# Kernel optimization log

Hardware: AMD Instinct MI355X
Metric: run time of the kernel (lower is better)

## Reference

```python
import jax, jax.numpy as jnp
import numpy as np

N = 100000
E = 6400000
GAMMA = 1.0
SUPPORT = 0.05


def cohesion_kernel(q, h):
    # piecewise Akinci cohesion kernel (Cd normalization is unused in the original)
    qm1_3_q3 = (q - 1.0) ** 3 * q ** 3
    k1 = 128.0 * qm1_3_q3 + 1.0   # q <= 0.5
    k2 = 64.0 * qm1_3_q3           # q > 0.5
    return -jnp.where(q <= 0.5, k1, k2)


def kernel_gradient(q, dist, h):
    # 2D Wendland C2 kernel gradient: W = 7/(pi h^2) (1-q)^4 (1+4q)
    C = 7.0 / (np.pi * h ** 2)
    dWdq = C * (-20.0 * q * jnp.clip(1.0 - q, 0.0, None) ** 3) / h
    return dWdq[:, None] * dist  # [E,2]


def setup_inputs() -> dict:
    key = jax.random.key(0)
    k1, k2, k3, k4, k5, k6, k7 = jax.random.split(key, 7)
    neighbors = jnp.stack([
        jax.random.randint(k1, (E,), 0, N),
        jax.random.randint(k2, (E,), 0, N),
    ], axis=0)  # [2,E] int
    fluidAreas = jax.random.uniform(k3, (N,), dtype=jnp.float32)
    fluidDensities = jax.random.uniform(k4, (N,), dtype=jnp.float32) + 0.5  # avoid div-by-0
    fluidRestDensity = jax.random.uniform(k5, (N,), dtype=jnp.float32) + 0.5
    fluidRadialDistances = jax.random.uniform(k6, (E,), dtype=jnp.float32)  # q in [0,1]
    fluidDistances = jax.random.normal(k7, (E, 2), dtype=jnp.float32)
    # normalize to unit direction vectors as in the SPH pipeline
    fluidDistances = fluidDistances / (jnp.linalg.norm(fluidDistances, axis=1, keepdims=True) + 1e-7)
    return {
        'neighbors': neighbors,
        'fluidAreas': fluidAreas,
        'fluidDensities': fluidDensities,
        'fluidRestDensity': fluidRestDensity,
        'fluidRadialDistances': fluidRadialDistances,
        'fluidDistances': fluidDistances,
    }


def reference(neighbors, fluidAreas, fluidDensities, fluidRestDensity,
              fluidRadialDistances, fluidDistances):
    i = neighbors[0]
    j = neighbors[1]

    # computeNormalFunction
    fac_n = fluidAreas[j] / fluidDensities[j]                  # [E]
    grad = kernel_gradient(fluidRadialDistances, fluidDistances, SUPPORT)  # [E,2]
    normals = SUPPORT * jax.ops.segment_sum(fac_n[:, None] * grad, i, num_segments=N)  # [N,2]

    # computeCurvatureForce
    curvature = -GAMMA * jax.ops.segment_sum(normals[i] - normals[j], i, num_segments=N)

    # computeCohesionForce
    fac_c = fluidAreas[j] * fluidRestDensity[j]                # [E]
    kern = cohesion_kernel(fluidRadialDistances, SUPPORT)      # [E]
    cohesion = -GAMMA * jax.ops.segment_sum((fac_c * kern)[:, None] * fluidDistances, i, num_segments=N)

    # both forces are accumulated into fluidAcceleration
    return curvature + cohesion
```

## Files before the change

### kernel.cpp

```cpp
#include <hip/hip_runtime.h>

constexpr int N_PART = 100000;
constexpr int N_EDGE = 6400000;
constexpr float SUPPORT = 0.05f;
constexpr float PI_F = 3.14159265358979323846f;

constexpr int CH_LOG2 = 12;
constexpr int CH      = 1 << CH_LOG2;
constexpr int NCH     = (N_EDGE + CH - 1) / CH;
constexpr int BIN_LOG2 = 13;
constexpr int BINSZ   = 1 << BIN_LOG2;
constexpr int NBIN    = (N_PART + BINSZ - 1) / BINSZ;
constexpr int G_MAX   = 39;
constexpr int ST_NW   = 8;

__global__ __launch_bounds__(512) void l1_sort(
    const int* __restrict__ nb,
    const float* __restrict__ areas,
    const float* __restrict__ dens,
    const float* __restrict__ rest,
    const float* __restrict__ q,
    const float2* __restrict__ dist,
    unsigned* __restrict__ gpack,
    float2* __restrict__ gpay1,
    float2* __restrict__ gpay2,
    unsigned* __restrict__ btab)
{
    __shared__ unsigned rec_pack[CH];
    __shared__ float    rec_q[CH];
    __shared__ float    rec_dx[CH];
    __shared__ float    rec_dy[CH];
    __shared__ unsigned hist[ST_NW * NBIN];
    __shared__ unsigned curw[ST_NW * NBIN];
    __shared__ unsigned base[NBIN + 1];

    const int t   = blockIdx.x;
    const int c0  = t * CH;
    const int len = min(CH, N_EDGE - c0);
    const int tid = threadIdx.x;
    const int wid = tid >> 6;

    for (int k = tid; k < ST_NW * NBIN; k += 512) hist[k] = 0u;
    __syncthreads();

    for (int idx = tid; idx < len; idx += 512) {
        unsigned i = (unsigned)nb[c0 + idx];
        atomicAdd(&hist[wid * NBIN + (i >> BIN_LOG2)], 1u);
    }
    __syncthreads();

    if (tid == 0) {
        unsigned run = 0;
        for (int b = 0; b < NBIN; ++b) {
            base[b] = run;
            for (int w = 0; w < ST_NW; ++w) {
                curw[w * NBIN + b] = run;
                run += hist[w * NBIN + b];
            }
        }
        base[NBIN] = run;
    }
    __syncthreads();
    if (tid < NBIN)  btab[t * 16 + tid]  = base[tid];
    if (tid == NBIN) btab[t * 16 + NBIN] = (unsigned)len;

    for (int idx = tid; idx < len; idx += 512) {
        unsigned i = (unsigned)nb[c0 + idx];
        unsigned j = (unsigned)nb[N_EDGE + c0 + idx];
        float   qq = q[c0 + idx];
        float2  d  = dist[c0 + idx];
        unsigned bin = i >> BIN_LOG2;
        unsigned r = atomicAdd(&curw[wid * NBIN + bin], 1u) & (CH - 1);
        rec_pack[r] = ((i & (BINSZ - 1)) << 17) | j;
        rec_q[r]    = qq;
        rec_dx[r]   = d.x;
        rec_dy[r]   = d.y;
    }
    __syncthreads();

    const float Cw = 7.0f / (PI_F * SUPPORT * SUPPORT);
    for (int p = tid; p < len; p += 512) {
        unsigned pack = rec_pack[p];
        float qq = rec_q[p];
        float dx = rec_dx[p], dy = rec_dy[p];
        unsigned j = pack & 0x1FFFFu;

        float omq  = fmaxf(1.0f - qq, 0.0f);
        float dWdq = Cw * (-20.0f * qq * omq * omq * omq) * (1.0f / SUPPORT);
        float s    = SUPPORT * (areas[j] / dens[j]) * dWdq;

        float qm1  = qq - 1.0f;
        float tt   = qm1 * qm1 * qm1 * qq * qq * qq;
        float kern = (qq <= 0.5f) ? fmaf(128.0f, tt, 1.0f) : 64.0f * tt;
        float fc   = areas[j] * rest[j] * kern;

        int o = c0 + p;
        gpack[o] = pack;
        gpay1[o] = make_float2(s * dx, s * dy);
        gpay2[o] = make_float2(fc * dx, fc * dy);
    }
}

__global__ __launch_bounds__(512) void passB(
    const unsigned* __restrict__ btab,
    const unsigned* __restrict__ gpack,
    const float2* __restrict__ gpay1,
    float2* __restrict__ partials,
    int G)
{
    __shared__ float accx[BINSZ];
    __shared__ float accy[BINSZ];
    const int b = blockIdx.x % NBIN;
    const int g = blockIdx.x / NBIN;
    const int wave = threadIdx.x >> 6;
    const int lane = threadIdx.x & 63;

    for (int k = threadIdx.x; k < BINSZ; k += 512) { accx[k] = 0.0f; accy[k] = 0.0f; }
    __syncthreads();

    const int t0 = (int)((long long)g * NCH / G);
    const int t1 = (int)((long long)(g + 1) * NCH / G);
    for (int t = t0 + wave; t < t1; t += 8) {
        const int c0  = t * CH;
        const unsigned ln = min(btab[t * 16 + NBIN], (unsigned)CH);
        unsigned sb = min(btab[t * 16 + b], ln);
        unsigned se = min(btab[t * 16 + b + 1], ln);
        for (unsigned k = sb + lane; k < se; k += 64) {
            int o = c0 + (int)k;
            unsigned pk = gpack[o];
            float2 p = gpay1[o];
            unsigned loc = (pk >> 17) & (BINSZ - 1);
            atomicAdd(&accx[loc], p.x);
            atomicAdd(&accy[loc], p.y);
        }
    }
    __syncthreads();

    float2* __restrict__ dst = partials + (size_t)g * (NBIN * BINSZ) + (size_t)b * BINSZ;
    for (int k = threadIdx.x; k < BINSZ; k += 512)
        dst[k] = make_float2(accx[k], accy[k]);
}

__global__ __launch_bounds__(512) void passD(
    const unsigned* __restrict__ btab,
    const unsigned* __restrict__ gpack,
    const float2* __restrict__ gpay2,
    const float2* __restrict__ normals,
    float2* __restrict__ partials,
    int G)
{
    __shared__ float accx[BINSZ];
    __shared__ float accy[BINSZ];
    const int b = blockIdx.x % NBIN;
    const int g = blockIdx.x / NBIN;
    const int wave = threadIdx.x >> 6;
    const int lane = threadIdx.x & 63;

    for (int k = threadIdx.x; k < BINSZ; k += 512) { accx[k] = 0.0f; accy[k] = 0.0f; }
    __syncthreads();

    const int gbase = b * BINSZ;
    const int t0 = (int)((long long)g * NCH / G);
    const int t1 = (int)((long long)(g + 1) * NCH / G);
    for (int t = t0 + wave; t < t1; t += 8) {
        const int c0  = t * CH;
        const unsigned ln = min(btab[t * 16 + NBIN], (unsigned)CH);
        unsigned sb = min(btab[t * 16 + b], ln);
        unsigned se = min(btab[t * 16 + b + 1], ln);
        for (unsigned k = sb + lane; k < se; k += 64) {
            int o = c0 + (int)k;
            unsigned pk = gpack[o];
            float2 coh = gpay2[o];
            unsigned loc = (pk >> 17) & (BINSZ - 1);
            unsigned j   = min(pk & 0x1FFFFu, (unsigned)(N_PART - 1));
            unsigned ii  = min((unsigned)(gbase + loc), (unsigned)(N_PART - 1));
            float2 nj = normals[j];
            float2 ni = normals[ii];
            atomicAdd(&accx[loc], nj.x - ni.x + coh.x);
            atomicAdd(&accy[loc], nj.y - ni.y + coh.y);
        }
    }
    __syncthreads();

    float2* __restrict__ dst = partials + (size_t)g * (NBIN * BINSZ) + (size_t)b * BINSZ;
    for (int k = threadIdx.x; k < BINSZ; k += 512)
        dst[k] = make_float2(accx[k], accy[k]);
}

__global__ __launch_bounds__(256) void reduceG(
    const float2* __restrict__ partials, float2* __restrict__ dst, int G)
{
    int p = blockIdx.x * blockDim.x + threadIdx.x;
    if (p >= N_PART) return;
    float ax = 0.0f, ay = 0.0f;
    for (int g = 0; g < G; ++g) {
        float2 v = partials[(size_t)g * (NBIN * BINSZ) + p];
        ax += v.x; ay += v.y;
    }
    dst[p] = make_float2(ax, ay);
}

constexpr int FB_BSZ_LOG2 = 13;
constexpr int FB_BSZ   = 1 << FB_BSZ_LOG2;
constexpr int FB_NBINS = (N_PART + FB_BSZ - 1) / FB_BSZ;
constexpr int FB_NP_PAD = FB_NBINS * FB_BSZ;
constexpr int FB_C_TARGET = 39;

__global__ __launch_bounds__(1024) void fb_pass1_binned(
    const int* __restrict__ nb, const float* __restrict__ areas,
    const float* __restrict__ dens, const float* __restrict__ q,
    const float2* __restrict__ dist, float* __restrict__ partials, int C)
{
    __shared__ float lds[2 * FB_BSZ];
    const int b = blockIdx.x % FB_NBINS;
    const int c = blockIdx.x / FB_NBINS;
    for (int k = threadIdx.x; k < 2 * FB_BSZ; k += blockDim.x) lds[k] = 0.0f;
    __syncthreads();
    const int start = (int)((long long)c       * (N_EDGE / 4) / C) * 4;
    const int end   = (int)((long long)(c + 1) * (N_EDGE / 4) / C) * 4;
    const int4* __restrict__ nb4 = (const int4*)nb;
    const float Cw = 7.0f / (PI_F * SUPPORT * SUPPORT);
    for (int e = start + (int)threadIdx.x * 4; e < end; e += (int)blockDim.x * 4) {
        int4 iq = nb4[e >> 2];
        #pragma unroll
        for (int k = 0; k < 4; ++k) {
            int iv = (k == 0) ? iq.x : (k == 1) ? iq.y : (k == 2) ? iq.z : iq.w;
            if ((iv >> FB_BSZ_LOG2) == b) {
                int ee = e + k;
                int j  = nb[N_EDGE + ee];
                float qq  = q[ee];
                float fac = areas[j] / dens[j];
                float omq  = fmaxf(1.0f - qq, 0.0f);
                float dWdq = Cw * (-20.0f * qq * omq * omq * omq) * (1.0f / SUPPORT);
                float s = SUPPORT * fac * dWdq;
                float2 d = dist[ee];
                int loc = (iv & (FB_BSZ - 1)) << 1;
                atomicAdd(&lds[loc],     s * d.x);
                atomicAdd(&lds[loc + 1], s * d.y);
            }
        }
    }
    __syncthreads();
    float2* __restrict__ dst = (float2*)partials + (size_t)c * FB_NP_PAD + (size_t)b * FB_BSZ;
    const float2* __restrict__ src = (const float2*)lds;
    for (int k = threadIdx.x; k < FB_BSZ; k += blockDim.x) dst[k] = src[k];
}

__global__ __launch_bounds__(1024) void fb_pass2_binned(
    const int* __restrict__ nb, const float* __restrict__ areas,
    const float* __restrict__ rest, const float* __restrict__ q,
    const float2* __restrict__ dist, const float2* __restrict__ normals,
    float* __restrict__ partials, int C)
{
    __shared__ float lds[2 * FB_BSZ];
    const int b = blockIdx.x % FB_NBINS;
    const int c = blockIdx.x / FB_NBINS;
    for (int k = threadIdx.x; k < 2 * FB_BSZ; k += blockDim.x) lds[k] = 0.0f;
    __syncthreads();
    const int start = (int)((long long)c       * (N_EDGE / 4) / C) * 4;
    const int end   = (int)((long long)(c + 1) * (N_EDGE / 4) / C) * 4;
    const int4* __restrict__ nb4 = (const int4*)nb;
    for (int e = start + (int)threadIdx.x * 4; e < end; e += (int)blockDim.x * 4) {
        int4 iq = nb4[e >> 2];
        #pragma unroll
        for (int k = 0; k < 4; ++k) {
            int iv = (k == 0) ? iq.x : (k == 1) ? iq.y : (k == 2) ? iq.z : iq.w;
            if ((iv >> FB_BSZ_LOG2) == b) {
                int ee = e + k;
                int j  = nb[N_EDGE + ee];
                float2 ni = normals[iv];
                float2 nj = normals[j];
                float qq  = q[ee];
                float fc  = areas[j] * rest[j];
                float qm1 = qq - 1.0f;
                float t   = qm1 * qm1 * qm1 * qq * qq * qq;
                float kern = (qq <= 0.5f) ? fmaf(128.0f, t, 1.0f) : 64.0f * t;
                float2 d = dist[ee];
                int loc = (iv & (FB_BSZ - 1)) << 1;
                atomicAdd(&lds[loc],     -(ni.x - nj.x) + fc * kern * d.x);
                atomicAdd(&lds[loc + 1], -(ni.y - nj.y) + fc * kern * d.y);
            }
        }
    }
    __syncthreads();
    float2* __restrict__ dst = (float2*)partials + (size_t)c * FB_NP_PAD + (size_t)b * FB_BSZ;
    const float2* __restrict__ src = (const float2*)lds;
    for (int k = threadIdx.x; k < FB_BSZ; k += blockDim.x) dst[k] = src[k];
}

__global__ __launch_bounds__(256) void fb_reduce_partials(
    const float* __restrict__ partials, float* __restrict__ dst, int C)
{
    int p = blockIdx.x * blockDim.x + threadIdx.x;
    if (p >= N_PART) return;
    const float2* __restrict__ p2 = (const float2*)partials;
    float ax = 0.0f, ay = 0.0f;
    for (int c = 0; c < C; ++c) {
        float2 v = p2[(size_t)c * FB_NP_PAD + p];
        ax += v.x; ay += v.y;
    }
    ((float2*)dst)[p] = make_float2(ax, ay);
}

__global__ __launch_bounds__(256) void fb_zero2(float* __restrict__ a,
                                                float* __restrict__ b, int n) {
    int idx = blockIdx.x * blockDim.x + threadIdx.x;
    if (idx < n) { a[idx] = 0.0f; b[idx] = 0.0f; }
}

__global__ __launch_bounds__(256) void fb_pass1_atomic(
    const int* __restrict__ nb, const float* __restrict__ areas,
    const float* __restrict__ dens, const float* __restrict__ q,
    const float2* __restrict__ dist, float* __restrict__ normals)
{
    int e = blockIdx.x * blockDim.x + threadIdx.x;
    if (e >= N_EDGE) return;
    int i = nb[e];
    int j = nb[N_EDGE + e];
    float qq  = q[e];
    float fac = areas[j] / dens[j];
    const float Cw = 7.0f / (PI_F * SUPPORT * SUPPORT);
    float omq  = fmaxf(1.0f - qq, 0.0f);
    float dWdq = Cw * (-20.0f * qq * omq * omq * omq) * (1.0f / SUPPORT);
    float s = SUPPORT * fac * dWdq;
    float2 d = dist[e];
    atomicAdd(&normals[2 * i],     s * d.x);
    atomicAdd(&normals[2 * i + 1], s * d.y);
}

__global__ __launch_bounds__(256) void fb_pass2_atomic(
    const int* __restrict__ nb, const float* __restrict__ areas,
    const float* __restrict__ rest, const float* __restrict__ q,
    const float2* __restrict__ dist, const float2* __restrict__ normals,
    float* __restrict__ out)
{
    int e = blockIdx.x * blockDim.x + threadIdx.x;
    if (e >= N_EDGE) return;
    int i = nb[e];
    int j = nb[N_EDGE + e];
    float2 ni = normals[i];
    float2 nj = normals[j];
    float qq  = q[e];
    float fc  = areas[j] * rest[j];
    float qm1 = qq - 1.0f;
    float t   = qm1 * qm1 * qm1 * qq * qq * qq;
    float kern = (qq <= 0.5f) ? fmaf(128.0f, t, 1.0f) : 64.0f * t;
    float2 d = dist[e];
    atomicAdd(&out[2 * i],     -(ni.x - nj.x) + fc * kern * d.x);
    atomicAdd(&out[2 * i + 1], -(ni.y - nj.y) + fc * kern * d.y);
}

extern "C" void kernel_launch(void* const* d_in, const int* in_sizes, int n_in,
                              void* d_out, int out_size, void* d_ws, size_t ws_size,
                              hipStream_t stream) {
    const int*   nb    = (const int*)d_in[0];
    const float* areas = (const float*)d_in[1];
    const float* dens  = (const float*)d_in[2];
    const float* rest  = (const float*)d_in[3];
    const float* q     = (const float*)d_in[4];
    const float* dist  = (const float*)d_in[5];
    float* out = (float*)d_out;

    size_t off = 0;
    auto take = [&](size_t bytes) { size_t o = off; off += (bytes + 255) & ~(size_t)255; return o; };
    size_t o_pack    = take((size_t)N_EDGE * sizeof(unsigned));
    size_t o_pay1    = take((size_t)N_EDGE * sizeof(float2));
    size_t o_pay2    = take((size_t)N_EDGE * sizeof(float2));
    size_t o_btab    = take((size_t)NCH * 16 * sizeof(unsigned));
    size_t o_normals = take((size_t)N_PART * sizeof(float2));
    size_t base_need = off;
    const size_t per_g = (size_t)(NBIN * BINSZ) * sizeof(float2);

    int G = 0;
    if (ws_size > base_need) {
        G = (int)((ws_size - base_need) / per_g);
        if (G > G_MAX) G = G_MAX;
    }

    char* ws = (char*)d_ws;

    if (G >= 6) {
        unsigned* gpack   = (unsigned*)(ws + o_pack);
        float2*   gpay1   = (float2*)(ws + o_pay1);
        float2*   gpay2   = (float2*)(ws + o_pay2);
        unsigned* btab    = (unsigned*)(ws + o_btab);
        float2*   normals = (float2*)(ws + o_normals);
        float2*   partials= (float2*)(ws + base_need);

        l1_sort<<<NCH, 512, 0, stream>>>(
            nb, areas, dens, rest, q, (const float2*)dist,
            gpack, gpay1, gpay2, btab);
        passB<<<NBIN * G, 512, 0, stream>>>(btab, gpack, gpay1, partials, G);
        reduceG<<<(N_PART + 255) / 256, 256, 0, stream>>>(partials, normals, G);
        passD<<<NBIN * G, 512, 0, stream>>>(btab, gpack, gpay2, normals, partials, G);
        reduceG<<<(N_PART + 255) / 256, 256, 0, stream>>>(partials, (float2*)out, G);
        return;
    }

    const size_t normals_pad = 1 << 20;
    float* normals  = (float*)d_ws;
    float* partials = (float*)((char*)d_ws + normals_pad);
    const size_t per_chunk = (size_t)FB_NP_PAD * 2 * sizeof(float);
    int C = 0;
    if (ws_size > normals_pad) {
        C = (int)((ws_size - normals_pad) / per_chunk);
        if (C > FB_C_TARGET) C = FB_C_TARGET;
    }

    if (C >= 4) {
        const int grid = FB_NBINS * C;
        fb_pass1_binned<<<grid, 1024, 0, stream>>>(
            nb, areas, dens, q, (const float2*)dist, partials, C);
        fb_reduce_partials<<<(N_PART + 255) / 256, 256, 0, stream>>>(partials, normals, C);
        fb_pass2_binned<<<grid, 1024, 0, stream>>>(
            nb, areas, rest, q, (const float2*)dist, (const float2*)normals, partials, C);
        fb_reduce_partials<<<(N_PART + 255) / 256, 256, 0, stream>>>(partials, out, C);
    } else {
        const int nv = 2 * N_PART;
        fb_zero2<<<(nv + 255) / 256, 256, 0, stream>>>(normals, out, nv);
        const int blocks = (N_EDGE + 255) / 256;
        fb_pass1_atomic<<<blocks, 256, 0, stream>>>(
            nb, areas, dens, q, (const float2*)dist, normals);
        fb_pass2_atomic<<<blocks, 256, 0, stream>>>(
            nb, areas, rest, q, (const float2*)dist, (const float2*)normals, out);
    }
}
```

Before: 432.1 us.

## Batch loads in register arrays across sort and accumulation passes for memory-level parallelism

The sort kernel now runs 256 threads over 2048-edge chunks with a fixed 8 edges per thread. It loads indices, payloads and gathered particle attributes into register arrays before using them, so many loads are in flight at once. PassB and passD are unrolled 4x so that packed records, payloads and normal gathers are all issued before the shared-memory atomics. Halving the chunk size doubles the number of chunks and btab entries scanned by the later passes. The code also assumes E divides the chunk size exactly and drops the tail handling.

```diff
diff --git a/kernel.cpp b/kernel.cpp
--- a/kernel.cpp
+++ b/kernel.cpp
@@ -5,16 +5,17 @@
 constexpr float SUPPORT = 0.05f;
 constexpr float PI_F = 3.14159265358979323846f;
 
-constexpr int CH_LOG2 = 12;
+constexpr int CH_LOG2 = 11;
 constexpr int CH      = 1 << CH_LOG2;
-constexpr int NCH     = (N_EDGE + CH - 1) / CH;
+constexpr int NCH     = N_EDGE / CH;
 constexpr int BIN_LOG2 = 13;
 constexpr int BINSZ   = 1 << BIN_LOG2;
 constexpr int NBIN    = (N_PART + BINSZ - 1) / BINSZ;
 constexpr int G_MAX   = 39;
-constexpr int ST_NW   = 8;
-
-__global__ __launch_bounds__(512) void l1_sort(
+constexpr int ST_NW   = 4;
+constexpr int E_PER   = CH / 256;
+
+__global__ __launch_bounds__(256) void l1_sort(
     const int* __restrict__ nb,
     const float* __restrict__ areas,
     const float* __restrict__ dens,
@@ -36,17 +37,19 @@
 
     const int t   = blockIdx.x;
     const int c0  = t * CH;
-    const int len = min(CH, N_EDGE - c0);
     const int tid = threadIdx.x;
     const int wid = tid >> 6;
 
-    for (int k = tid; k < ST_NW * NBIN; k += 512) hist[k] = 0u;
-    __syncthreads();
-
-    for (int idx = tid; idx < len; idx += 512) {
-        unsigned i = (unsigned)nb[c0 + idx];
-        atomicAdd(&hist[wid * NBIN + (i >> BIN_LOG2)], 1u);
-    }
+    for (int k = tid; k < ST_NW * NBIN; k += 256) hist[k] = 0u;
+    __syncthreads();
+
+    unsigned iv[E_PER];
+    #pragma unroll
+    for (int k = 0; k < E_PER; ++k)
+        iv[k] = (unsigned)nb[c0 + tid + k * 256];
+    #pragma unroll
+    for (int k = 0; k < E_PER; ++k)
+        atomicAdd(&hist[wid * NBIN + (iv[k] >> BIN_LOG2)], 1u);
     __syncthreads();
 
     if (tid == 0) {
@@ -62,42 +65,59 @@
     }
     __syncthreads();
     if (tid < NBIN)  btab[t * 16 + tid]  = base[tid];
-    if (tid == NBIN) btab[t * 16 + NBIN] = (unsigned)len;
-
-    for (int idx = tid; idx < len; idx += 512) {
-        unsigned i = (unsigned)nb[c0 + idx];
-        unsigned j = (unsigned)nb[N_EDGE + c0 + idx];
-        float   qq = q[c0 + idx];
-        float2  d  = dist[c0 + idx];
-        unsigned bin = i >> BIN_LOG2;
+    if (tid == NBIN) btab[t * 16 + NBIN] = (unsigned)CH;
+
+    unsigned jv[E_PER];
+    float    qv[E_PER], dxv[E_PER], dyv[E_PER];
+    #pragma unroll
+    for (int k = 0; k < E_PER; ++k) {
+        int idx = tid + k * 256;
+        jv[k] = (unsigned)nb[N_EDGE + c0 + idx];
+        qv[k] = q[c0 + idx];
+        float2 d = dist[c0 + idx];
+        dxv[k] = d.x; dyv[k] = d.y;
+    }
+    #pragma unroll
+    for (int k = 0; k < E_PER; ++k) {
+        unsigned bin = iv[k] >> BIN_LOG2;
         unsigned r = atomicAdd(&curw[wid * NBIN + bin], 1u) & (CH - 1);
-        rec_pack[r] = ((i & (BINSZ - 1)) << 17) | j;
-        rec_q[r]    = qq;
-        rec_dx[r]   = d.x;
-        rec_dy[r]   = d.y;
+        rec_pack[r] = ((iv[k] & (BINSZ - 1)) << 17) | jv[k];
+        rec_q[r]    = qv[k];
+        rec_dx[r]   = dxv[k];
+        rec_dy[r]   = dyv[k];
     }
     __syncthreads();
 
     const float Cw = 7.0f / (PI_F * SUPPORT * SUPPORT);
-    for (int p = tid; p < len; p += 512) {
-        unsigned pack = rec_pack[p];
-        float qq = rec_q[p];
-        float dx = rec_dx[p], dy = rec_dy[p];
-        unsigned j = pack & 0x1FFFFu;
-
+    unsigned pk[E_PER]; float q3[E_PER], dx3[E_PER], dy3[E_PER];
+    float ar[E_PER], de[E_PER], re[E_PER];
+    #pragma unroll
+    for (int k = 0; k < E_PER; ++k) {
+        int p = tid + k * 256;
+        pk[k] = rec_pack[p];
+        q3[k] = rec_q[p]; dx3[k] = rec_dx[p]; dy3[k] = rec_dy[p];
+    }
+    #pragma unroll
+    for (int k = 0; k < E_PER; ++k) {
+        unsigned j = pk[k] & 0x1FFFFu;
+        ar[k] = areas[j]; de[k] = dens[j]; re[k] = rest[j];
+    }
+    #pragma unroll
+    for (int k = 0; k < E_PER; ++k) {
+        float qq = q3[k];
         float omq  = fmaxf(1.0f - qq, 0.0f);
         float dWdq = Cw * (-20.0f * qq * omq * omq * omq) * (1.0f / SUPPORT);
-        float s    = SUPPORT * (areas[j] / dens[j]) * dWdq;
+        float s    = SUPPORT * (ar[k] / de[k]) * dWdq;
 
         float qm1  = qq - 1.0f;
         float tt   = qm1 * qm1 * qm1 * qq * qq * qq;
         float kern = (qq <= 0.5f) ? fmaf(128.0f, tt, 1.0f) : 64.0f * tt;
-        float fc   = areas[j] * rest[j] * kern;
-
-        int o = c0 + p;
-        gpack[o] = pack;
-        gpay1[o] = make_float2(s * dx, s * dy);
-        gpay2[o] = make_float2(fc * dx, fc * dy);
+        float fc   = ar[k] * re[k] * kern;
+
+        int o = c0 + tid + k * 256;
+        gpack[o] = pk[k];
+        gpay1[o] = make_float2(s * dx3[k], s * dy3[k]);
+        gpay2[o] = make_float2(fc * dx3[k], fc * dy3[k]);
     }
 }
 
@@ -125,13 +145,25 @@
         const unsigned ln = min(btab[t * 16 + NBIN], (unsigned)CH);
         unsigned sb = min(btab[t * 16 + b], ln);
         unsigned se = min(btab[t * 16 + b + 1], ln);
-        for (unsigned k = sb + lane; k < se; k += 64) {
-            int o = c0 + (int)k;
-            unsigned pk = gpack[o];
-            float2 p = gpay1[o];
-            unsigned loc = (pk >> 17) & (BINSZ - 1);
-            atomicAdd(&accx[loc], p.x);
-            atomicAdd(&accy[loc], p.y);
+        for (unsigned k = sb + lane; k < se; k += 256) {
+            unsigned pkv[4]; float px[4], py[4];
+            #pragma unroll
+            for (int u = 0; u < 4; ++u) {
+                unsigned kk = k + (unsigned)(u * 64);
+                bool v = kk < se;
+                int o = c0 + (int)(v ? kk : k);
+                unsigned pw = gpack[o];
+                float2 p = gpay1[o];
+                pkv[u] = v ? pw : 0u;
+                px[u] = v ? p.x : 0.0f;
+                py[u] = v ? p.y : 0.0f;
+            }
+            #pragma unroll
+            for (int u = 0; u < 4; ++u) {
+                unsigned loc = (pkv[u] >> 17) & (BINSZ - 1);
+                atomicAdd(&accx[loc], px[u]);
+                atomicAdd(&accy[loc], py[u]);
+            }
         }
     }
     __syncthreads();
@@ -167,17 +199,37 @@
         const unsigned ln = min(btab[t * 16 + NBIN], (unsigned)CH);
         unsigned sb = min(btab[t * 16 + b], ln);
         unsigned se = min(btab[t * 16 + b + 1], ln);
-        for (unsigned k = sb + lane; k < se; k += 64) {
-            int o = c0 + (int)k;
-            unsigned pk = gpack[o];
-            float2 coh = gpay2[o];
-            unsigned loc = (pk >> 17) & (BINSZ - 1);
-            unsigned j   = min(pk & 0x1FFFFu, (unsigned)(N_PART - 1));
-            unsigned ii  = min((unsigned)(gbase + loc), (unsigned)(N_PART - 1));
-            float2 nj = normals[j];
-            float2 ni = normals[ii];
-            atomicAdd(&accx[loc], nj.x - ni.x + coh.x);
-            atomicAdd(&accy[loc], nj.y - ni.y + coh.y);
+        for (unsigned k = sb + lane; k < se; k += 256) {
+            unsigned pkv[4]; float cx[4], cy[4]; bool vv[4];
+            #pragma unroll
+            for (int u = 0; u < 4; ++u) {
+                unsigned kk = k + (unsigned)(u * 64);
+                bool v = kk < se;
+                int o = c0 + (int)(v ? kk : k);
+                unsigned pw = gpack[o];
+                float2 p = gpay2[o];
+                vv[u] = v;
+                pkv[u] = v ? pw : 0u;
+                cx[u] = p.x; cy[u] = p.y;
+            }
+            float njx[4], njy[4], nix[4], niy[4];
+            #pragma unroll
+            for (int u = 0; u < 4; ++u) {
+                unsigned loc = (pkv[u] >> 17) & (BINSZ - 1);
+                unsigned j   = min(pkv[u] & 0x1FFFFu, (unsigned)(N_PART - 1));
+                unsigned ii  = min((unsigned)(gbase + loc), (unsigned)(N_PART - 1));
+                float2 nj = normals[j];
+                float2 ni = normals[ii];
+                njx[u] = nj.x; njy[u] = nj.y; nix[u] = ni.x; niy[u] = ni.y;
+            }
+            #pragma unroll
+            for (int u = 0; u < 4; ++u) {
+                unsigned loc = (pkv[u] >> 17) & (BINSZ - 1);
+                float ax = vv[u] ? (njx[u] - nix[u] + cx[u]) : 0.0f;
+                float ay = vv[u] ? (njy[u] - niy[u] + cy[u]) : 0.0f;
+                atomicAdd(&accx[loc], ax);
+                atomicAdd(&accy[loc], ay);
+            }
         }
     }
     __syncthreads();
@@ -387,7 +439,7 @@
         float2*   normals = (float2*)(ws + o_normals);
         float2*   partials= (float2*)(ws + base_need);
 
-        l1_sort<<<NCH, 512, 0, stream>>>(
+        l1_sort<<<NCH, 256, 0, stream>>>(
             nb, areas, dens, rest, q, (const float2*)dist,
             gpack, gpay1, gpay2, btab);
         passB<<<NBIN * G, 512, 0, stream>>>(btab, gpack, gpay1, partials, G);
```

Result: slower. 475.9 us (+10.2%).
